# Kernel optimization log

Hardware: AMD Instinct MI355X
Metric: run time of the kernel (lower is better)

Reference implementation:

```python
import math
import jax, jax.numpy as jnp
import numpy as np

V, D, H, F, L = 32128, 768, 12, 3072, 12
NUM_BUCKETS, MAX_DIST = 32, 128
B, S = 16, 512
EPS = 1e-6


def _rel_bucket(rel_pos, num_buckets=NUM_BUCKETS, max_distance=MAX_DIST):
    # bidirectional T5 bucketing
    num_buckets //= 2
    ret = (rel_pos > 0).astype(jnp.int32) * num_buckets
    n = jnp.abs(rel_pos)
    max_exact = num_buckets // 2
    is_small = n < max_exact
    large = max_exact + (
        jnp.log(n.astype(jnp.float32) / max_exact)
        / math.log(max_distance / max_exact)
        * (num_buckets - max_exact)
    ).astype(jnp.int32)
    large = jnp.minimum(large, num_buckets - 1)
    return ret + jnp.where(is_small, n.astype(jnp.int32), large)


def t5_layernorm(x, w):
    # RMS norm: no mean subtraction, no bias
    var = jnp.mean(x * x, axis=-1, keepdims=True)
    return x * jax.lax.rsqrt(var + EPS) * w


def setup_inputs() -> dict:
    key = jax.random.key(0)
    ks = jax.random.split(key, 12)
    sc = 0.02
    inp = {
        "tokens": jax.random.randint(ks[0], (B, S), 0, V, dtype=jnp.int64),
        "emb": jax.random.normal(ks[1], (V, D), jnp.float32) * sc,
        "rel_bias": jax.random.normal(ks[2], (NUM_BUCKETS, H), jnp.float32) * sc,
        "ln1_w": jnp.ones((L, D), jnp.float32),
        "wq": jax.random.normal(ks[3], (L, D, D), jnp.float32) * sc,
        "wk": jax.random.normal(ks[4], (L, D, D), jnp.float32) * sc,
        "wv": jax.random.normal(ks[5], (L, D, D), jnp.float32) * sc,
        "wo": jax.random.normal(ks[6], (L, D, D), jnp.float32) * sc,
        "ln2_w": jnp.ones((L, D), jnp.float32),
        "w1": jax.random.normal(ks[7], (L, D, F), jnp.float32) * sc,
        "w2": jax.random.normal(ks[8], (L, F, D), jnp.float32) * sc,
        "ln_final_w": jnp.ones((D,), jnp.float32),
    }
    return inp


def _attn(x, pos_bias, wq, wk, wv, wo):
    b, s, d = x.shape
    dh = d // H
    q = (x @ wq).reshape(b, s, H, dh).transpose(0, 2, 1, 3)
    k = (x @ wk).reshape(b, s, H, dh).transpose(0, 2, 1, 3)
    v = (x @ wv).reshape(b, s, H, dh).transpose(0, 2, 1, 3)
    # T5: NO 1/sqrt(dh) scaling; add bucketed relative-position bias
    scores = jnp.einsum("bhqd,bhkd->bhqk", q, k) + pos_bias[None]  # [B,H,S,S]
    a = jax.nn.softmax(scores, axis=-1)
    o = jnp.einsum("bhqk,bhkd->bhqd", a, v)
    o = o.transpose(0, 2, 1, 3).reshape(b, s, d)
    return o @ wo


def reference(tokens, emb, rel_bias, ln1_w, wq, wk, wv, wo, ln2_w, w1, w2, ln_final_w):
    x = emb[tokens]  # [B,S,D]
    s = tokens.shape[1]
    pos = jnp.arange(s)
    buckets = _rel_bucket(pos[None, :] - pos[:, None])  # [S,S]
    pos_bias = rel_bias[buckets].transpose(2, 0, 1)  # [H,S,S], computed once (layer 0)
    for i in range(L):
        h = t5_layernorm(x, ln1_w[i])
        x = x + _attn(h, pos_bias, wq[i], wk[i], wv[i], wo[i])
        h = t5_layernorm(x, ln2_w[i])
        x = x + jax.nn.relu(h @ w1[i]) @ w2[i]
    return t5_layernorm(x, ln_final_w)
```

## Files before the change

kernel.cpp:

```cpp
#include <hip/hip_runtime.h>
#include <hip/hip_bf16.h>

typedef unsigned short u16;
typedef unsigned int   u32;
typedef __attribute__((ext_vector_type(8))) __bf16 bf16x8;
typedef __attribute__((ext_vector_type(4))) float  f32x4;
typedef __attribute__((ext_vector_type(4))) u16    u16x4;
typedef __attribute__((ext_vector_type(4))) u32    u32x4;

#define SEQ     512
#define DMODEL  768
#define NHEAD   12
#define DHEAD   64
#define FDIM    3072
#define NLAYER  12
#define NROWS   8192
#define QKVN    2304

__device__ __forceinline__ u16 f2bf(float f) {
  union { float f; u32 u; } x; x.f = f;
  u32 r = x.u + 0x7fffu + ((x.u >> 16) & 1u);
  return (u16)(r >> 16);
}
__device__ __forceinline__ float u2f(u32 u) { union { u32 u; float f; } x; x.u = u; return x.f; }

__global__ __launch_bounds__(256) void k_transpose_cvt(const float* __restrict__ in,
                                                       u16* __restrict__ out, int K, int N,
                                                       size_t istride, size_t ostride) {
  __shared__ float tile[32][33];
  in  += (size_t)blockIdx.z * istride;
  out += (size_t)blockIdx.z * ostride;
  int nb = blockIdx.x * 32, kb = blockIdx.y * 32;
  int tx = threadIdx.x, ty = threadIdx.y;
#pragma unroll
  for (int i = 0; i < 4; i++)
    tile[ty + 8 * i][tx] = in[(size_t)(kb + ty + 8 * i) * N + nb + tx];
  __syncthreads();
#pragma unroll
  for (int i = 0; i < 4; i++)
    out[(size_t)(nb + ty + 8 * i) * K + kb + tx] = f2bf(tile[tx][ty + 8 * i]);
}

__global__ __launch_bounds__(256) void k_embed(const int* __restrict__ tokens,
                                               const float* __restrict__ emb,
                                               float* __restrict__ x) {
  int idx = blockIdx.x * 256 + threadIdx.x;
  int row = idx / 192, c4 = idx % 192;
  int tok = tokens[row];
  reinterpret_cast<float4*>(x + (size_t)row * DMODEL)[c4] =
      reinterpret_cast<const float4*>(emb + (size_t)tok * DMODEL)[c4];
}

__global__ __launch_bounds__(256) void k_biaslut(const float* __restrict__ rel_bias,
                                                 float* __restrict__ lut) {
  int idx = blockIdx.x * 256 + threadIdx.x;
  int h = idx >> 10, i = idx & 1023;
  int rel = i - 511;
  int ret = rel > 0 ? 16 : 0;
  int n = rel < 0 ? -rel : rel;
  int b;
  if (n < 8) {
    b = n;
  } else {
    float r = logf((float)n * 0.125f) / 2.772588722239781f * 8.0f;
    int lg = 8 + (int)r;
    b = lg < 15 ? lg : 15;
  }
  b += ret;
  lut[idx] = rel_bias[b * NHEAD + h];
}

template <int BF16OUT>
__global__ __launch_bounds__(256) void k_rmsnorm(const float* __restrict__ x,
                                                 const float* __restrict__ w,
                                                 void* __restrict__ out) {
  int row = blockIdx.x * 4 + (threadIdx.x >> 6);
  int lane = threadIdx.x & 63;
  const float4* xr = reinterpret_cast<const float4*>(x + (size_t)row * DMODEL);
  float4 a = xr[lane], b = xr[lane + 64], c = xr[lane + 128];
  float ss = a.x * a.x + a.y * a.y + a.z * a.z + a.w * a.w
           + b.x * b.x + b.y * b.y + b.z * b.z + b.w * b.w
           + c.x * c.x + c.y * c.y + c.z * c.z + c.w * c.w;
#pragma unroll
  for (int off = 1; off < 64; off <<= 1) ss += __shfl_xor(ss, off);
  float sc = rsqrtf(ss * (1.0f / 768.0f) + 1e-6f);
  const float4* wr = reinterpret_cast<const float4*>(w);
  float4 w0 = wr[lane], w1 = wr[lane + 64], w2 = wr[lane + 128];
  if (BF16OUT) {
    u16x4* o = reinterpret_cast<u16x4*>((u16*)out + (size_t)row * DMODEL);
    u16x4 v0, v1, v2;
    v0[0] = f2bf(a.x * sc * w0.x); v0[1] = f2bf(a.y * sc * w0.y);
    v0[2] = f2bf(a.z * sc * w0.z); v0[3] = f2bf(a.w * sc * w0.w);
    v1[0] = f2bf(b.x * sc * w1.x); v1[1] = f2bf(b.y * sc * w1.y);
    v1[2] = f2bf(b.z * sc * w1.z); v1[3] = f2bf(b.w * sc * w1.w);
    v2[0] = f2bf(c.x * sc * w2.x); v2[1] = f2bf(c.y * sc * w2.y);
    v2[2] = f2bf(c.z * sc * w2.z); v2[3] = f2bf(c.w * sc * w2.w);
    o[lane] = v0; o[lane + 64] = v1; o[lane + 128] = v2;
  } else {
    float4* o = reinterpret_cast<float4*>((float*)out + (size_t)row * DMODEL);
    float4 v0, v1, v2;
    v0.x = a.x * sc * w0.x; v0.y = a.y * sc * w0.y; v0.z = a.z * sc * w0.z; v0.w = a.w * sc * w0.w;
    v1.x = b.x * sc * w1.x; v1.y = b.y * sc * w1.y; v1.z = b.z * sc * w1.z; v1.w = b.w * sc * w1.w;
    v2.x = c.x * sc * w2.x; v2.y = c.y * sc * w2.y; v2.z = c.z * sc * w2.z; v2.w = c.w * sc * w2.w;
    o[lane] = v0; o[lane + 64] = v1; o[lane + 128] = v2;
  }
}

__device__ __forceinline__ void gload_lds16(const void* g, void* l) {
  __builtin_amdgcn_global_load_lds((const __attribute__((address_space(1))) void*)g,
                                   (__attribute__((address_space(3))) void*)l, 16, 0, 0);
}

template <int EPI>
__global__ __launch_bounds__(512, 2) void k_gemm(const u16* __restrict__ A, const u16* __restrict__ Bt,
                                                 u16* __restrict__ outb, float* __restrict__ outf,
                                                 int M, int N, int K) {
  __shared__ u16 lds[3 * 24576];
  const int NT = K >> 6;
  int tid = threadIdx.x;
  int lane = tid & 63, wid = tid >> 6;
  int lr = lane & 15, lh = lane >> 4;
  int wm = wid >> 1, wn = wid & 1;

  int gx = gridDim.x;
  int gm = gridDim.y;
  int nwg = gx * gm;
  int linear = blockIdx.y * gx + blockIdx.x;
  int cpx = nwg >> 3;
  int swz = (linear & 7) * cpx + (linear >> 3);
  int bm = (swz % gm) * 256;
  int bn = (swz / gm) * 128;

  const u16* Ab = A  + (size_t)bm * K;
  const u16* Bb = Bt + (size_t)bn * K;

  int cswz = (((tid & 3) ^ ((tid >> 2) & 3) ^ ((tid >> 4) & 3))) * 8;
  int arow = tid >> 2;

  f32x4 acc[4][4] = {};

  auto STAGE_A = [&](int kt, u16* dst) {
#pragma unroll
    for (int a = 0; a < 4; a++) {
      const u16* src = Ab + (size_t)((a & 1) * 128 + arow) * K + kt * 64 + (a >> 1) * 32 + cswz;
      gload_lds16(src, dst + a * 4096 + (size_t)tid * 8);
    }
  };
  auto STAGE_B = [&](int kt, u16* dst) {
#pragma unroll
    for (int b = 0; b < 2; b++) {
      const u16* src = Bb + (size_t)arow * K + kt * 64 + b * 32 + cswz;
      gload_lds16(src, dst + 16384 + b * 4096 + (size_t)tid * 8);
    }
  };

  STAGE_A(0, lds);
  STAGE_B(0, lds);
  STAGE_A(1, lds + 24576);
  STAGE_B(1, lds + 24576);
  asm volatile("s_waitcnt vmcnt(6)" ::: "memory");
  __builtin_amdgcn_s_barrier();

  bf16x8 af[4], bfr[4];
  int rsw = ((lr & 3) ^ ((lr >> 2) & 3)) * 8;
  int chunk = (lh * 8) ^ rsw;

#define DSA(KK)                                                                 \
  _Pragma("unroll") for (int i = 0; i < 4; i++) {                               \
    int row = wm * 64 + i * 16 + lr;                                            \
    af[i] = *reinterpret_cast<const bf16x8*>(cur + (KK) * 8192 + row * 32 + chunk); \
  }
#define DSB(KK)                                                                 \
  _Pragma("unroll") for (int n = 0; n < 4; n++) {                               \
    int row = wn * 64 + n * 16 + lr;                                            \
    bfr[n] = *reinterpret_cast<const bf16x8*>(cur + 16384 + (KK) * 4096 + row * 32 + chunk); \
  }
#define MFMA16                                                                  \
  __builtin_amdgcn_s_setprio(1);                                                \
  _Pragma("unroll") for (int i = 0; i < 4; i++)                                 \
  _Pragma("unroll") for (int n = 0; n < 4; n++)                                 \
    acc[i][n] = __builtin_amdgcn_mfma_f32_16x16x32_bf16(af[i], bfr[n], acc[i][n], 0, 0, 0); \
  __builtin_amdgcn_s_setprio(0);
#define BAR_LGKM                                                                \
  __builtin_amdgcn_s_barrier();                                                 \
  asm volatile("s_waitcnt lgkmcnt(0)" ::: "memory");                            \
  __builtin_amdgcn_sched_barrier(0);

  int cur_s = 0;
  for (int t = 0; t < NT; ++t) {
    const u16* cur = lds + cur_s * 24576;
    int dst_s = cur_s + 2; if (dst_s >= 3) dst_s -= 3;
    u16* dst = lds + dst_s * 24576;
    int t2 = (t + 2 < NT) ? t + 2 : t + 2 - NT;

    DSA(0)
    DSB(0)
    STAGE_A(t2, dst);
    BAR_LGKM
    MFMA16
    __builtin_amdgcn_s_barrier();

    DSA(1)
    DSB(1)
    STAGE_B(t2, dst);
    BAR_LGKM
    MFMA16
    asm volatile("s_waitcnt vmcnt(6)" ::: "memory");
    __builtin_amdgcn_s_barrier();

    cur_s += 1; if (cur_s >= 3) cur_s -= 3;
  }
#undef DSA
#undef DSB
#undef MFMA16
#undef BAR_LGKM

#pragma unroll
  for (int i = 0; i < 4; i++)
#pragma unroll
    for (int n = 0; n < 4; n++)
#pragma unroll
      for (int r = 0; r < 4; r++) {
        int row = bm + wm * 64 + i * 16 + lh * 4 + r;
        int col = bn + wn * 64 + n * 16 + lr;
        size_t idx = (size_t)row * N + col;
        float v = acc[i][n][r];
        if (EPI == 0)      outb[idx] = f2bf(v);
        else if (EPI == 1) outb[idx] = f2bf(v > 0.f ? v : 0.f);
        else               outf[idx] += v;
      }
}

__global__ __launch_bounds__(256) void k_vtrans(const u16* __restrict__ qkv, u16* __restrict__ vt) {
  __shared__ u16 t[32][33];
  int bh = blockIdx.z;
  int b = bh / NHEAD, h = bh % NHEAD;
  int d0 = blockIdx.x * 32, s0 = blockIdx.y * 32;
  int tx = threadIdx.x, ty = threadIdx.y;
  const u16* src = qkv + (size_t)(b * SEQ + s0) * QKVN + 2 * DMODEL + h * DHEAD + d0;
#pragma unroll
  for (int i = 0; i < 4; i++)
    t[ty + 8 * i][tx] = src[(size_t)(ty + 8 * i) * QKVN + tx];
  __syncthreads();
  u16* dst = vt + ((size_t)bh * DHEAD + d0) * SEQ + s0;
#pragma unroll
  for (int i = 0; i < 4; i++)
    dst[(size_t)(ty + 8 * i) * SEQ + tx] = t[tx][ty + 8 * i];
}

__global__ __launch_bounds__(256) void k_attn(const u16* __restrict__ qkv,
                                              const u16* __restrict__ vt,
                                              const float* __restrict__ lutg,
                                              u16* __restrict__ ob) {
  __shared__ __align__(16) float lut[1024];
  __shared__ __align__(16) u16 Ks[2][4096];
  __shared__ __align__(16) u16 Vs[2][4096];
  __shared__ __align__(16) u16 Ps[4][2048];
  int b = blockIdx.x / NHEAD, h = blockIdx.x % NHEAD;
  int qt = blockIdx.y;
  int tid = threadIdx.x;
  int lane = tid & 63, wid = tid >> 6;
  int lr = lane & 15, lh = lane >> 4;
  int q0 = qt * 128 + wid * 32;

  reinterpret_cast<float4*>(lut)[tid] = reinterpret_cast<const float4*>(lutg + h * 1024)[tid];

  bf16x8 aq[2][2];
#pragma unroll
  for (int m = 0; m < 2; m++) {
    const u16* qp = qkv + (size_t)(b * SEQ + q0 + m * 16 + lr) * QKVN + h * DHEAD;
#pragma unroll
    for (int kk = 0; kk < 2; kk++)
      aq[m][kk] = *reinterpret_cast<const bf16x8*>(qp + kk * 32 + lh * 8);
  }

  float mrun[2][4], lpart[2][4];
  f32x4 acc_o[2][4] = {};
#pragma unroll
  for (int m = 0; m < 2; m++)
#pragma unroll
    for (int r = 0; r < 4; r++) { mrun[m][r] = -3.0e38f; lpart[m][r] = 0.f; }

  int srow = tid >> 3, sc8 = tid & 7;
  int scs = (sc8 ^ (srow & 7)) << 3;
  const u16* kbase = qkv + (size_t)(b * SEQ + srow) * QKVN + DMODEL + h * DHEAD + scs;
  const u16* vbase = vt + ((size_t)blockIdx.x * DHEAD + srow) * SEQ + scs;

  auto STAGE = [&](int kt, int bufi) {
    int kv0 = kt << 6;
    gload_lds16(kbase + (size_t)kv0 * QKVN,        &Ks[bufi][tid * 8]);
    gload_lds16(kbase + (size_t)(kv0 + 32) * QKVN, &Ks[bufi][2048 + tid * 8]);
    gload_lds16(vbase + kv0,                       &Vs[bufi][tid * 8]);
    gload_lds16(vbase + 32 * SEQ + kv0,            &Vs[bufi][2048 + tid * 8]);
  };

  STAGE(0, 0);
  asm volatile("s_waitcnt vmcnt(0) lgkmcnt(0)" ::: "memory");
  __builtin_amdgcn_s_barrier();

  int ibase = 511 + lr - q0 - lh * 4;
  u16* pw = Ps[wid];

  for (int kt = 0; kt < 8; kt++) {
    int cb = kt & 1;
    __builtin_amdgcn_s_barrier();
    STAGE((kt + 1) & 7, cb ^ 1);
    asm volatile("s_waitcnt vmcnt(4)" ::: "memory");
    __builtin_amdgcn_s_barrier();

    const u16* KsC = Ks[cb];
    const u16* VsC = Vs[cb];
    int kv0 = kt << 6;

    f32x4 sc[2][4] = {};
#pragma unroll
    for (int kk = 0; kk < 2; kk++) {
      bf16x8 bk[4];
#pragma unroll
      for (int n = 0; n < 4; n++) {
        int row = n * 16 + lr;
        int c = (kk * 4 + lh) ^ (lr & 7);
        bk[n] = *reinterpret_cast<const bf16x8*>(KsC + row * 64 + c * 8);
      }
#pragma unroll
      for (int m = 0; m < 2; m++)
#pragma unroll
        for (int n = 0; n < 4; n++)
          sc[m][n] = __builtin_amdgcn_mfma_f32_16x16x32_bf16(aq[m][kk], bk[n], sc[m][n], 0, 0, 0);
    }

    int pred = 1;
    float vmax[2][4];
#pragma unroll
    for (int m = 0; m < 2; m++)
#pragma unroll
      for (int r = 0; r < 4; r++) {
        int ib = ibase + kv0 - m * 16 - r;
#pragma unroll
        for (int n = 0; n < 4; n++)
          sc[m][n][r] += lut[ib + n * 16];
        float v = fmaxf(fmaxf(sc[m][0][r], sc[m][1][r]), fmaxf(sc[m][2][r], sc[m][3][r]));
        v = fmaxf(v, __shfl_xor(v, 1));
        v = fmaxf(v, __shfl_xor(v, 2));
        v = fmaxf(v, __shfl_xor(v, 4));
        v = fmaxf(v, __shfl_xor(v, 8));
        vmax[m][r] = v;
        pred = pred && (v <= mrun[m][r] + 8.0f);
      }
    if (!__all(pred)) {
#pragma unroll
      for (int m = 0; m < 2; m++)
#pragma unroll
        for (int r = 0; r < 4; r++) {
          float mo = mrun[m][r];
          float mn = fmaxf(mo, vmax[m][r]);
          float corr = __expf(mo - mn);
          mrun[m][r] = mn;
          lpart[m][r] *= corr;
#pragma unroll
          for (int n = 0; n < 4; n++) acc_o[m][n][r] *= corr;
        }
    }
#pragma unroll
    for (int m = 0; m < 2; m++)
#pragma unroll
      for (int r = 0; r < 4; r++) {
        float mm = mrun[m][r];
        int prow = m * 16 + lh * 4 + r;
        int pbse = prow * 64;
        int sw = prow & 7;
        float lp = lpart[m][r];
#pragma unroll
        for (int n = 0; n < 4; n++) {
          float pv = __expf(sc[m][n][r] - mm);
          lp += pv;
          pw[pbse + ((((n << 1) | (lr >> 3)) ^ sw) << 3) + (lr & 7)] = f2bf(pv);
        }
        lpart[m][r] = lp;
      }

    asm volatile("s_waitcnt lgkmcnt(0)" ::: "memory");
    __builtin_amdgcn_sched_barrier(0);
#pragma unroll
    for (int kk = 0; kk < 2; kk++) {
      bf16x8 bvv[4], ap[2];
#pragma unroll
      for (int n = 0; n < 4; n++) {
        int row = n * 16 + lr;
        int c = (kk * 4 + lh) ^ (lr & 7);
        bvv[n] = *reinterpret_cast<const bf16x8*>(VsC + row * 64 + c * 8);
      }
#pragma unroll
      for (int m = 0; m < 2; m++) {
        int row = m * 16 + lr;
        int c = (kk * 4 + lh) ^ (lr & 7);
        ap[m] = *reinterpret_cast<const bf16x8*>(pw + row * 64 + c * 8);
      }
#pragma unroll
      for (int m = 0; m < 2; m++)
#pragma unroll
        for (int n = 0; n < 4; n++)
          acc_o[m][n] = __builtin_amdgcn_mfma_f32_16x16x32_bf16(ap[m], bvv[n], acc_o[m][n], 0, 0, 0);
    }
  }

#pragma unroll
  for (int m = 0; m < 2; m++)
#pragma unroll
    for (int r = 0; r < 4; r++) {
      float l = lpart[m][r];
      l += __shfl_xor(l, 1);
      l += __shfl_xor(l, 2);
      l += __shfl_xor(l, 4);
      l += __shfl_xor(l, 8);
      float inv = 1.f / l;
      size_t orow = (size_t)(b * SEQ + q0 + m * 16 + lh * 4 + r);
#pragma unroll
      for (int n = 0; n < 4; n++)
        ob[orow * DMODEL + h * DHEAD + n * 16 + lr] = f2bf(acc_o[m][n][r] * inv);
    }
}

extern "C" void kernel_launch(void* const* d_in, const int* in_sizes, int n_in,
                              void* d_out, int out_size, void* d_ws, size_t ws_size,
                              hipStream_t stream) {
  const int*   tokens = (const int*)  d_in[0];
  const float* emb    = (const float*)d_in[1];
  const float* relb   = (const float*)d_in[2];
  const float* ln1w   = (const float*)d_in[3];
  const float* wq     = (const float*)d_in[4];
  const float* wk     = (const float*)d_in[5];
  const float* wv     = (const float*)d_in[6];
  const float* wo     = (const float*)d_in[7];
  const float* ln2w   = (const float*)d_in[8];
  const float* w1     = (const float*)d_in[9];
  const float* w2     = (const float*)d_in[10];
  const float* lnfw   = (const float*)d_in[11];
  float* out = (float*)d_out;

  char* p = (char*)d_ws;
  auto carve = [&](size_t bytes) { char* r = p; p += (bytes + 255) & ~(size_t)255; return r; };
  const size_t DD = (size_t)DMODEL * DMODEL, DF = (size_t)DMODEL * FDIM;

  u16*   wqkv_t = (u16*)carve(NLAYER * 3 * DD * 2);
  u16*   wo_t   = (u16*)carve(NLAYER * DD * 2);
  u16*   w1_t   = (u16*)carve(NLAYER * DF * 2);
  u16*   w2_t   = (u16*)carve(NLAYER * DF * 2);
  float* x      = (float*)carve((size_t)NROWS * DMODEL * 4);
  u16*   hbuf   = (u16*)carve((size_t)NROWS * DMODEL * 2);
  u16*   qkvbuf = (u16*)carve((size_t)NROWS * QKVN * 2);
  u16*   abuf   = (u16*)carve((size_t)NROWS * DMODEL * 2);
  u16*   fbuf   = (u16*)carve((size_t)NROWS * FDIM * 2);
  float* lutbuf = (float*)carve((size_t)NHEAD * 1024 * 4);
  u16*   vtbuf  = fbuf;

  dim3 tb(32, 8);
  k_transpose_cvt<<<dim3(24, 24, NLAYER), tb, 0, stream>>>(wq, wqkv_t,          DMODEL, DMODEL, DD, 3 * DD);
  k_transpose_cvt<<<dim3(24, 24, NLAYER), tb, 0, stream>>>(wk, wqkv_t + DD,     DMODEL, DMODEL, DD, 3 * DD);
  k_transpose_cvt<<<dim3(24, 24, NLAYER), tb, 0, stream>>>(wv, wqkv_t + 2 * DD, DMODEL, DMODEL, DD, 3 * DD);
  k_transpose_cvt<<<dim3(24, 24, NLAYER), tb, 0, stream>>>(wo, wo_t,            DMODEL, DMODEL, DD, DD);
  k_transpose_cvt<<<dim3(96, 24, NLAYER), tb, 0, stream>>>(w1, w1_t,            DMODEL, FDIM,   DF, DF);
  k_transpose_cvt<<<dim3(24, 96, NLAYER), tb, 0, stream>>>(w2, w2_t,            FDIM, DMODEL,   DF, DF);

  k_embed<<<NROWS * 192 / 256, 256, 0, stream>>>(tokens, emb, x);
  k_biaslut<<<48, 256, 0, stream>>>(relb, lutbuf);

  for (int i = 0; i < NLAYER; i++) {
    k_rmsnorm<1><<<NROWS / 4, 256, 0, stream>>>(x, ln1w + i * DMODEL, hbuf);
    k_gemm<0><<<dim3(18, 32), 512, 0, stream>>>(hbuf, wqkv_t + (size_t)i * 3 * DD, qkvbuf, nullptr, NROWS, QKVN, DMODEL);
    k_vtrans<<<dim3(2, 16, 192), tb, 0, stream>>>(qkvbuf, vtbuf);
    k_attn<<<dim3(192, 4), 256, 0, stream>>>(qkvbuf, vtbuf, lutbuf, abuf);
    k_gemm<2><<<dim3(6, 32),  512, 0, stream>>>(abuf, wo_t + (size_t)i * DD, nullptr, x, NROWS, DMODEL, DMODEL);
    k_rmsnorm<1><<<NROWS / 4, 256, 0, stream>>>(x, ln2w + i * DMODEL, hbuf);
    k_gemm<1><<<dim3(24, 32), 512, 0, stream>>>(hbuf, w1_t + (size_t)i * DF, fbuf, nullptr, NROWS, FDIM, DMODEL);
    k_gemm<2><<<dim3(6, 32),  512, 0, stream>>>(fbuf, w2_t + (size_t)i * DF, nullptr, x, NROWS, DMODEL, FDIM);
  }
  k_rmsnorm<0><<<NROWS / 4, 256, 0, stream>>>(x, lnfw, out);
}
```

Measured before the change: 3.602 ms.

## Rework GEMM LDS tile layout to 64-wide rows with XOR swizzle and N-major block order

Changes the GEMM's LDS tile layout from two 32-column halves to full 64-element rows with an XOR-by-row chunk swizzle, and stages global loads to match. B fragments for both k-halves are now loaded once at the start of each iteration, so B reads no longer sit in the second phase. The block swizzle now maps tiles N-fastest instead of M-fastest, which changes L2 reuse patterns. The aim is fewer LDS bank conflicts and better cache locality, at the cost of more registers held for B fragments.

```diff
diff --git a/kernel.cpp b/kernel.cpp
--- a/kernel.cpp
+++ b/kernel.cpp
@@ -6,7 +6,6 @@
 typedef __attribute__((ext_vector_type(8))) __bf16 bf16x8;
 typedef __attribute__((ext_vector_type(4))) float  f32x4;
 typedef __attribute__((ext_vector_type(4))) u16    u16x4;
-typedef __attribute__((ext_vector_type(4))) u32    u32x4;
 
 #define SEQ     512
 #define DMODEL  768
@@ -22,7 +21,6 @@
   u32 r = x.u + 0x7fffu + ((x.u >> 16) & 1u);
   return (u16)(r >> 16);
 }
-__device__ __forceinline__ float u2f(u32 u) { union { u32 u; float f; } x; x.u = u; return x.f; }
 
 __global__ __launch_bounds__(256) void k_transpose_cvt(const float* __restrict__ in,
                                                        u16* __restrict__ out, int K, int N,
@@ -122,35 +120,35 @@
   int lr = lane & 15, lh = lane >> 4;
   int wm = wid >> 1, wn = wid & 1;
 
-  int gx = gridDim.x;
-  int gm = gridDim.y;
+  int gx = gridDim.x, gm = gridDim.y;
   int nwg = gx * gm;
   int linear = blockIdx.y * gx + blockIdx.x;
   int cpx = nwg >> 3;
   int swz = (linear & 7) * cpx + (linear >> 3);
-  int bm = (swz % gm) * 256;
-  int bn = (swz / gm) * 128;
+  int bn = (swz % gx) * 128;
+  int bm = (swz / gx) * 256;
 
   const u16* Ab = A  + (size_t)bm * K;
   const u16* Bb = Bt + (size_t)bn * K;
 
-  int cswz = (((tid & 3) ^ ((tid >> 2) & 3) ^ ((tid >> 4) & 3))) * 8;
-  int arow = tid >> 2;
-
   f32x4 acc[4][4] = {};
 
-  auto STAGE_A = [&](int kt, u16* dst) {
-#pragma unroll
-    for (int a = 0; a < 4; a++) {
-      const u16* src = Ab + (size_t)((a & 1) * 128 + arow) * K + kt * 64 + (a >> 1) * 32 + cswz;
-      gload_lds16(src, dst + a * 4096 + (size_t)tid * 8);
+  auto STAGE_A = [&](int kt, u16* buf) {
+#pragma unroll
+    for (int i = 0; i < 4; i++) {
+      int elem = i * 512 + tid;
+      int row = elem >> 3, ch = elem & 7;
+      int chs = ch ^ (row & 7);
+      gload_lds16(Ab + (size_t)row * K + kt * 64 + chs * 8, buf + elem * 8);
     }
   };
-  auto STAGE_B = [&](int kt, u16* dst) {
-#pragma unroll
-    for (int b = 0; b < 2; b++) {
-      const u16* src = Bb + (size_t)arow * K + kt * 64 + b * 32 + cswz;
-      gload_lds16(src, dst + 16384 + b * 4096 + (size_t)tid * 8);
+  auto STAGE_B = [&](int kt, u16* buf) {
+#pragma unroll
+    for (int i = 0; i < 2; i++) {
+      int elem = i * 512 + tid;
+      int row = elem >> 3, ch = elem & 7;
+      int chs = ch ^ (row & 7);
+      gload_lds16(Bb + (size_t)row * K + kt * 64 + chs * 8, buf + 16384 + elem * 8);
     }
   };
 
@@ -161,57 +159,54 @@
   asm volatile("s_waitcnt vmcnt(6)" ::: "memory");
   __builtin_amdgcn_s_barrier();
 
-  bf16x8 af[4], bfr[4];
-  int rsw = ((lr & 3) ^ ((lr >> 2) & 3)) * 8;
-  int chunk = (lh * 8) ^ rsw;
+  bf16x8 af[4], bfr[2][4];
 
 #define DSA(KK)                                                                 \
   _Pragma("unroll") for (int i = 0; i < 4; i++) {                               \
-    int row = wm * 64 + i * 16 + lr;                                            \
-    af[i] = *reinterpret_cast<const bf16x8*>(cur + (KK) * 8192 + row * 32 + chunk); \
-  }
-#define DSB(KK)                                                                 \
-  _Pragma("unroll") for (int n = 0; n < 4; n++) {                               \
-    int row = wn * 64 + n * 16 + lr;                                            \
-    bfr[n] = *reinterpret_cast<const bf16x8*>(cur + 16384 + (KK) * 4096 + row * 32 + chunk); \
-  }
-#define MFMA16                                                                  \
+    int r = wm * 64 + i * 16 + lr;                                              \
+    af[i] = *reinterpret_cast<const bf16x8*>(cur + r * 64 + ((((KK) * 4 + lh) ^ (r & 7)) * 8)); \
+  }
+#define MFMA16(KK)                                                              \
   __builtin_amdgcn_s_setprio(1);                                                \
   _Pragma("unroll") for (int i = 0; i < 4; i++)                                 \
   _Pragma("unroll") for (int n = 0; n < 4; n++)                                 \
-    acc[i][n] = __builtin_amdgcn_mfma_f32_16x16x32_bf16(af[i], bfr[n], acc[i][n], 0, 0, 0); \
+    acc[i][n] = __builtin_amdgcn_mfma_f32_16x16x32_bf16(af[i], bfr[KK][n], acc[i][n], 0, 0, 0); \
   __builtin_amdgcn_s_setprio(0);
 #define BAR_LGKM                                                                \
   __builtin_amdgcn_s_barrier();                                                 \
   asm volatile("s_waitcnt lgkmcnt(0)" ::: "memory");                            \
   __builtin_amdgcn_sched_barrier(0);
 
-  int cur_s = 0;
+  int cs = 0;
   for (int t = 0; t < NT; ++t) {
-    const u16* cur = lds + cur_s * 24576;
-    int dst_s = cur_s + 2; if (dst_s >= 3) dst_s -= 3;
-    u16* dst = lds + dst_s * 24576;
-    int t2 = (t + 2 < NT) ? t + 2 : t + 2 - NT;
-
+    const u16* cur = lds + cs * 24576;
+    int ds = cs + 2; if (ds >= 3) ds -= 3;
+    u16* dst = lds + ds * 24576;
+    int t2 = t + 2; if (t2 >= NT) t2 -= NT;
+
+#pragma unroll
+    for (int kk = 0; kk < 2; kk++)
+#pragma unroll
+      for (int n = 0; n < 4; n++) {
+        int r = wn * 64 + n * 16 + lr;
+        bfr[kk][n] = *reinterpret_cast<const bf16x8*>(cur + 16384 + r * 64 + (((kk * 4 + lh) ^ (r & 7)) * 8));
+      }
     DSA(0)
-    DSB(0)
     STAGE_A(t2, dst);
     BAR_LGKM
-    MFMA16
+    MFMA16(0)
     __builtin_amdgcn_s_barrier();
 
     DSA(1)
-    DSB(1)
     STAGE_B(t2, dst);
     BAR_LGKM
-    MFMA16
+    MFMA16(1)
     asm volatile("s_waitcnt vmcnt(6)" ::: "memory");
     __builtin_amdgcn_s_barrier();
 
-    cur_s += 1; if (cur_s >= 3) cur_s -= 3;
+    cs += 1; if (cs >= 3) cs -= 3;
   }
 #undef DSA
-#undef DSB
 #undef MFMA16
 #undef BAR_LGKM
 
@@ -467,13 +462,17 @@
 
   for (int i = 0; i < NLAYER; i++) {
     k_rmsnorm<1><<<NROWS / 4, 256, 0, stream>>>(x, ln1w + i * DMODEL, hbuf);
-    k_gemm<0><<<dim3(18, 32), 512, 0, stream>>>(hbuf, wqkv_t + (size_t)i * 3 * DD, qkvbuf, nullptr, NROWS, QKVN, DMODEL);
+    k_gemm<0><<<dim3(18, 32), 512, 0, stream>>>(hbuf, wqkv_t + (size_t)i * 3 * DD, qkvbuf, nullptr,
+                                                NROWS, QKVN, DMODEL);
     k_vtrans<<<dim3(2, 16, 192), tb, 0, stream>>>(qkvbuf, vtbuf);
     k_attn<<<dim3(192, 4), 256, 0, stream>>>(qkvbuf, vtbuf, lutbuf, abuf);
-    k_gemm<2><<<dim3(6, 32),  512, 0, stream>>>(abuf, wo_t + (size_t)i * DD, nullptr, x, NROWS, DMODEL, DMODEL);
+    k_gemm<2><<<dim3(6, 32),  512, 0, stream>>>(abuf, wo_t + (size_t)i * DD, nullptr, x,
+                                                NROWS, DMODEL, DMODEL);
     k_rmsnorm<1><<<NROWS / 4, 256, 0, stream>>>(x, ln2w + i * DMODEL, hbuf);
-    k_gemm<1><<<dim3(24, 32), 512, 0, stream>>>(hbuf, w1_t + (size_t)i * DF, fbuf, nullptr, NROWS, FDIM, DMODEL);
-    k_gemm<2><<<dim3(6, 32),  512, 0, stream>>>(fbuf, w2_t + (size_t)i * DF, nullptr, x, NROWS, DMODEL, FDIM);
+    k_gemm<1><<<dim3(24, 32), 512, 0, stream>>>(hbuf, w1_t + (size_t)i * DF, fbuf, nullptr,
+                                                NROWS, FDIM, DMODEL);
+    k_gemm<2><<<dim3(6, 32),  512, 0, stream>>>(fbuf, w2_t + (size_t)i * DF, nullptr, x,
+                                                NROWS, DMODEL, FDIM);
   }
   k_rmsnorm<0><<<NROWS / 4, 256, 0, stream>>>(x, lnfw, out);
 }
```

Result: faster. 3.273 ms (-9.1%).
